# Kernel optimization log

Measured on AMD Instinct MI355X. Metric: run time of the kernel, lower is better.

The kernel has to match this reference:

```python
import jax, jax.numpy as jnp
import numpy as np

N, E, IN, H, OUT = 50000, 1600000, 128, 128, 16


def setup_inputs() -> dict:
    key = jax.random.key(0)
    ks = jax.random.split(key, 8)
    return {
        "x": jax.random.normal(ks[0], (N, IN), dtype=jnp.float32),
        "edge_index": jax.random.randint(ks[1], (2, E), 0, N, dtype=jnp.int64),
        "W1": jax.random.normal(ks[2], (IN, H), dtype=jnp.float32) * 0.05,
        "b1": jax.random.normal(ks[3], (H,), dtype=jnp.float32) * 0.05,
        "W2": jax.random.normal(ks[4], (H, H), dtype=jnp.float32) * 0.05,
        "b2": jax.random.normal(ks[5], (H,), dtype=jnp.float32) * 0.05,
        "Wc": jax.random.normal(ks[6], (H, OUT), dtype=jnp.float32) * 0.05,
        "bc": jax.random.normal(ks[7], (OUT,), dtype=jnp.float32) * 0.05,
    }


def _gcn_conv(x, src, dst, norm, W, b, n):
    # PyG GCNConv: h = x @ W; out[i] = sum_{(j->i)} norm_e * h[j]; out += b
    h = x @ W
    msg = h[src] * norm[:, None]          # [E+N, H] gather + scale
    out = jax.ops.segment_sum(msg, dst, num_segments=n)  # scatter-add
    return out + b


def reference(x, edge_index, W1, b1, W2, b2, Wc, bc):
    n = x.shape[0]
    loop = jnp.arange(n, dtype=edge_index.dtype)
    src = jnp.concatenate([edge_index[0], loop])  # add self-loops
    dst = jnp.concatenate([edge_index[1], loop])
    # symmetric normalization: deg over destinations (incl. self-loops)
    deg = jnp.zeros((n,), dtype=x.dtype).at[dst].add(1.0)
    d_inv_sqrt = jnp.where(deg > 0, jax.lax.rsqrt(deg), 0.0)
    norm = d_inv_sqrt[src] * d_inv_sqrt[dst]
    h = jax.nn.relu(_gcn_conv(x, src, dst, norm, W1, b1, n))
    # dropout p=0.5 is identity in eval mode
    h = jax.nn.relu(_gcn_conv(h, src, dst, norm, W2, b2, n))
    return h @ Wc + bc
```

## Files before the change

### kernel.cpp

```cpp
#include <hip/hip_runtime.h>
#include <hip/hip_bf16.h>


typedef unsigned int uint;
typedef unsigned short ushort;
typedef __attribute__((ext_vector_type(8))) short bf16x8;
typedef __attribute__((ext_vector_type(4))) float f32x4;

#define NPB 256
#define MAXBKT 256
#define CAP 12288

static __device__ __forceinline__ ushort f2bf(float f) {
    unsigned u = __float_as_uint(f);
    u += 0x7fffu + ((u >> 16) & 1u);
    return (ushort)(u >> 16);
}
static __device__ __forceinline__ uint pack2(float a, float b) {
    return (uint)f2bf(a) | ((uint)f2bf(b) << 16);
}
static __device__ __forceinline__ float lo2f(uint u) { return __uint_as_float(u << 16); }
static __device__ __forceinline__ float hi2f(uint u) { return __uint_as_float(u & 0xffff0000u); }

#define UNPACK8(dst, u)                                        \
    dst[0] = lo2f(u.x); dst[1] = hi2f(u.x);                    \
    dst[2] = lo2f(u.y); dst[3] = hi2f(u.y);                    \
    dst[4] = lo2f(u.z); dst[5] = hi2f(u.z);                    \
    dst[6] = lo2f(u.w); dst[7] = hi2f(u.w);


__global__ __launch_bounds__(256) void initcur(int* __restrict__ bcursor, int nbuckets) {
    int t = threadIdx.x;
    if (t < nbuckets) bcursor[t] = t * CAP;
}

__global__ __launch_bounds__(256) void bin_edges(const int* __restrict__ src,
                                                 const int* __restrict__ dst,
                                                 int* __restrict__ bcursor,
                                                 uint* __restrict__ pay,
                                                 int E, int nbuckets) {
    __shared__ int h[MAXBKT];
    __shared__ int base[MAXBKT];
    int tid = threadIdx.x;
    h[tid] = 0;
    __syncthreads();
    int chunk = (E + gridDim.x - 1) / gridDim.x;
    int i0 = blockIdx.x * chunk;
    int i1 = min(E, i0 + chunk);
    for (int i = i0 + tid; i < i1; i += 256) atomicAdd(&h[dst[i] >> 8], 1);
    __syncthreads();
    if (tid < nbuckets) base[tid] = h[tid] ? atomicAdd(&bcursor[tid], h[tid]) : 0;
    __syncthreads();
    h[tid] = 0;
    __syncthreads();
    for (int i = i0 + tid; i < i1; i += 256) {
        int d = dst[i];
        int b = d >> 8;
        int pos = base[b] + atomicAdd(&h[b], 1);
        pay[pos] = (uint)src[i] | ((uint)(d & 255) << 24);
    }
}

__global__ __launch_bounds__(256) void build_rows(const uint* __restrict__ pay,
                                                  const int* __restrict__ bcursor,
                                                  int* __restrict__ rowstart,
                                                  int* __restrict__ rowend,
                                                  float* __restrict__ dinv,
                                                  int* __restrict__ colidx, int n) {
    __shared__ int hist[NPB];
    __shared__ int sc[NPB];
    __shared__ int cur[NPB];
    int tid = threadIdx.x;
    int b = blockIdx.x;
    int node0 = b * NPB;
    int s = b * CAP, e = bcursor[b];

    hist[tid] = 0;
    __syncthreads();
    for (int i = s + tid; i < e; i += 256) atomicAdd(&hist[pay[i] >> 24], 1);
    __syncthreads();

    int v = hist[tid];
    sc[tid] = v;
    __syncthreads();
    for (int d = 1; d < 256; d <<= 1) {
        int x = (tid >= d) ? sc[tid - d] : 0;
        __syncthreads();
        sc[tid] += x;
        __syncthreads();
    }
    int excl = sc[tid] - v;
    cur[tid] = s + excl;
    int node = node0 + tid;
    if (node < n) {
        rowstart[node] = s + excl;
        rowend[node] = s + excl + v;
        dinv[node] = rsqrtf((float)(v + 1));
    }
    __syncthreads();

    for (int i = s + tid; i < e; i += 256) {
        uint p = pay[i];
        int pos = atomicAdd(&cur[p >> 24], 1);
        colidx[pos] = (int)(p & 0xffffffu);
    }
}

__global__ __launch_bounds__(256) void prep_wt(const float* __restrict__ W1,
                                               const float* __restrict__ W2,
                                               ushort* __restrict__ Wt1,
                                               ushort* __restrict__ Wt2) {
    int idx = blockIdx.x * 256 + threadIdx.x;
    int k = idx >> 7, nn = idx & 127;
    Wt1[nn * 128 + k] = f2bf(W1[idx]);
    Wt2[nn * 128 + k] = f2bf(W2[idx]);
}

template <bool A_BF16>
__global__ __launch_bounds__(256) void gemm_mfma(const void* __restrict__ Xv,
                                                 const ushort* __restrict__ Wt,
                                                 const float* __restrict__ dinv,
                                                 uint* __restrict__ Yb, int n) {
    __shared__ __align__(16) ushort sOut[4][16][136];
    const int wave = threadIdx.x >> 6;
    const int lane = threadIdx.x & 63;
    const int quad = lane >> 4, l16 = lane & 15;
    const int m0 = blockIdx.x * 64 + wave * 16;

    f32x4 acc[8];
#pragma unroll
    for (int t = 0; t < 8; ++t) acc[t] = (f32x4){0.f, 0.f, 0.f, 0.f};

    int arow = m0 + l16;
    arow = arow < n ? arow : n - 1;

#pragma unroll
    for (int ks = 0; ks < 4; ++ks) {
        bf16x8 a;
        if (A_BF16) {
            const ushort* X = (const ushort*)Xv;
            a = *(const bf16x8*)&X[(size_t)arow * 128 + ks * 32 + quad * 8];
        } else {
            const float* X = (const float*)Xv;
            const float* px = &X[(size_t)arow * 128 + ks * 32 + quad * 8];
            float4 x0 = *(const float4*)px;
            float4 x1 = *(const float4*)(px + 4);
            ushort av[8] = {f2bf(x0.x), f2bf(x0.y), f2bf(x0.z), f2bf(x0.w),
                            f2bf(x1.x), f2bf(x1.y), f2bf(x1.z), f2bf(x1.w)};
            a = *(const bf16x8*)av;
        }
#pragma unroll
        for (int nt = 0; nt < 8; ++nt) {
            bf16x8 b = *(const bf16x8*)&Wt[(size_t)(nt * 16 + l16) * 128 + ks * 32 + quad * 8];
            acc[nt] = __builtin_amdgcn_mfma_f32_16x16x32_bf16(a, b, acc[nt], 0, 0, 0);
        }
    }

    float dv[4];
#pragma unroll
    for (int r = 0; r < 4; ++r) {
        int rr = m0 + quad * 4 + r;
        dv[r] = dinv[rr < n ? rr : n - 1];
    }
#pragma unroll
    for (int nt = 0; nt < 8; ++nt)
#pragma unroll
        for (int r = 0; r < 4; ++r)
            sOut[wave][quad * 4 + r][nt * 16 + l16] = f2bf(acc[nt][r] * dv[r]);
    __syncthreads();

#pragma unroll
    for (int i = 0; i < 4; ++i) {
        int linear = i * 64 + lane;
        int row = linear >> 4, chunk = linear & 15;
        int rr = m0 + row;
        if (rr < n) {
            uint4 v = *(const uint4*)&sOut[wave][row][chunk * 8];
            *(uint4*)&Yb[(size_t)rr * 64 + chunk * 4] = v;
        }
    }
}

static __device__ __forceinline__ void gather_q(const uint4* __restrict__ H4,
                                                int s, int e, int nn, int sub,
                                                const int* __restrict__ colidx,
                                                float acc[8]) {
    uint4 su = H4[(size_t)nn * 16 + sub];
    float t[8];
    UNPACK8(t, su);
#pragma unroll
    for (int j = 0; j < 8; ++j) acc[j] = t[j];

    int p = s;
    for (; p + 8 <= e; p += 8) {
        int c[8];
#pragma unroll
        for (int i = 0; i < 8; ++i) c[i] = colidx[p + i];
        uint4 u[8];
#pragma unroll
        for (int i = 0; i < 8; ++i) u[i] = H4[(size_t)c[i] * 16 + sub];
#pragma unroll
        for (int i = 0; i < 8; ++i) {
            float a[8];
            UNPACK8(a, u[i]);
#pragma unroll
            for (int j = 0; j < 8; ++j) acc[j] += a[j];
        }
    }
    if (p < e) {
        int c[8];
#pragma unroll
        for (int i = 0; i < 8; ++i) c[i] = (p + i < e) ? colidx[p + i] : nn;
        uint4 u[8];
#pragma unroll
        for (int i = 0; i < 8; ++i) u[i] = H4[(size_t)c[i] * 16 + sub];
#pragma unroll
        for (int i = 0; i < 8; ++i) {
            float a[8];
            UNPACK8(a, u[i]);
#pragma unroll
            for (int j = 0; j < 8; ++j) acc[j] += a[j];
        }
        float pad = (float)(p + 8 - e);
#pragma unroll
        for (int j = 0; j < 8; ++j) acc[j] -= pad * t[j];
    }
}

__global__ __launch_bounds__(256) void agg_mid_q(const uint4* __restrict__ H4,
                                                 const int* __restrict__ rowstart,
                                                 const int* __restrict__ rowend,
                                                 const int* __restrict__ colidx,
                                                 const float* __restrict__ dinv,
                                                 const float* __restrict__ bias,
                                                 uint4* __restrict__ Ob, int n) {
    int tid = threadIdx.x;
    int sub = tid & 15;
    int node = blockIdx.x * 16 + (tid >> 4);
    int nn = node < n ? node : n - 1;
    int s = rowstart[nn], e = rowend[nn];
    float di = dinv[nn];

    float acc[8];
    gather_q(H4, s, e, nn, sub, colidx, acc);

    if (node < n) {
        float4 b0 = ((const float4*)bias)[sub * 2];
        float4 b1 = ((const float4*)bias)[sub * 2 + 1];
        float o0 = fmaxf(fmaf(acc[0], di, b0.x), 0.f);
        float o1 = fmaxf(fmaf(acc[1], di, b0.y), 0.f);
        float o2 = fmaxf(fmaf(acc[2], di, b0.z), 0.f);
        float o3 = fmaxf(fmaf(acc[3], di, b0.w), 0.f);
        float o4 = fmaxf(fmaf(acc[4], di, b1.x), 0.f);
        float o5 = fmaxf(fmaf(acc[5], di, b1.y), 0.f);
        float o6 = fmaxf(fmaf(acc[6], di, b1.z), 0.f);
        float o7 = fmaxf(fmaf(acc[7], di, b1.w), 0.f);
        uint4 ov;
        ov.x = pack2(o0, o1); ov.y = pack2(o2, o3);
        ov.z = pack2(o4, o5); ov.w = pack2(o6, o7);
        Ob[(size_t)node * 16 + sub] = ov;
    }
}

__global__ __launch_bounds__(256) void agg_out_q(const uint4* __restrict__ H4,
                                                 const int* __restrict__ rowstart,
                                                 const int* __restrict__ rowend,
                                                 const int* __restrict__ colidx,
                                                 const float* __restrict__ dinv,
                                                 const float* __restrict__ bias,
                                                 const float* __restrict__ Wc,
                                                 const float* __restrict__ bc,
                                                 float* __restrict__ out, int n) {
    __shared__ float sA[16][129];
    int tid = threadIdx.x;
    int sub = tid & 15;
    int nl = tid >> 4;
    int node = blockIdx.x * 16 + nl;
    int nn = node < n ? node : n - 1;
    int s = rowstart[nn], e = rowend[nn];
    float di = dinv[nn];

    float acc[8];
    gather_q(H4, s, e, nn, sub, colidx, acc);

    {
        float4 b0 = ((const float4*)bias)[sub * 2];
        float4 b1 = ((const float4*)bias)[sub * 2 + 1];
        float f[8];
        f[0] = fmaxf(fmaf(acc[0], di, b0.x), 0.f);
        f[1] = fmaxf(fmaf(acc[1], di, b0.y), 0.f);
        f[2] = fmaxf(fmaf(acc[2], di, b0.z), 0.f);
        f[3] = fmaxf(fmaf(acc[3], di, b0.w), 0.f);
        f[4] = fmaxf(fmaf(acc[4], di, b1.x), 0.f);
        f[5] = fmaxf(fmaf(acc[5], di, b1.y), 0.f);
        f[6] = fmaxf(fmaf(acc[6], di, b1.z), 0.f);
        f[7] = fmaxf(fmaf(acc[7], di, b1.w), 0.f);
#pragma unroll
        for (int j = 0; j < 8; ++j) sA[nl][sub * 8 + j] = f[j];
    }
    __syncthreads();

    int col = tid & 15;
    float p0 = 0.f, p1 = 0.f;
#pragma unroll 4
    for (int k = 0; k < 128; k += 2) {
        p0 = fmaf(sA[nl][k], Wc[k * 16 + col], p0);
        p1 = fmaf(sA[nl][k + 1], Wc[(k + 1) * 16 + col], p1);
    }
    if (node < n) out[(size_t)node * 16 + col] = p0 + p1 + bc[col];
}


extern "C" void kernel_launch(void* const* d_in, const int* in_sizes, int n_in,
                              void* d_out, int out_size, void* d_ws, size_t ws_size,
                              hipStream_t stream) {
    const float* x  = (const float*)d_in[0];
    const int*   ei = (const int*)d_in[1];
    const float* W1 = (const float*)d_in[2];
    const float* b1 = (const float*)d_in[3];
    const float* W2 = (const float*)d_in[4];
    const float* b2 = (const float*)d_in[5];
    const float* Wc = (const float*)d_in[6];
    const float* bc = (const float*)d_in[7];
    float* out = (float*)d_out;

    const int n = in_sizes[0] / 128;
    const int E = in_sizes[1] / 2;
    const int* src = ei;
    const int* dst = ei + E;
    const int nbuckets = (n + NPB - 1) / NPB;

    char* p = (char*)d_ws;
    auto alloc = [&](size_t bytes) {
        char* q = p;
        p += (bytes + 255) & ~(size_t)255;
        return q;
    };
    int*    bcursor  = (int*)alloc(MAXBKT * 4);
    int*    rowstart = (int*)alloc((size_t)n * 4);
    int*    rowend   = (int*)alloc((size_t)n * 4);
    float*  dinv     = (float*)alloc((size_t)n * 4);
    ushort* Wt1      = (ushort*)alloc(128 * 128 * 2);
    ushort* Wt2      = (ushort*)alloc(128 * 128 * 2);
    uint*   pay      = (uint*)alloc((size_t)nbuckets * CAP * 4);
    int*    colidx   = (int*)alloc((size_t)nbuckets * CAP * 4);
    uint*   bufA     = (uint*)alloc((size_t)n * 64 * 4);
    uint*   bufB     = (uint*)alloc((size_t)n * 64 * 4);
    if ((size_t)(p - (char*)d_ws) > ws_size) return;

    initcur<<<1, 256, 0, stream>>>(bcursor, nbuckets);
    bin_edges<<<256, 256, 0, stream>>>(src, dst, bcursor, pay, E, nbuckets);
    build_rows<<<nbuckets, 256, 0, stream>>>(pay, bcursor, rowstart, rowend, dinv, colidx, n);
    prep_wt<<<64, 256, 0, stream>>>(W1, W2, Wt1, Wt2);

    const int gemmb = (n + 63) / 64;
    const int aggb = (n + 15) / 16;
    gemm_mfma<false><<<gemmb, 256, 0, stream>>>(x, Wt1, dinv, bufA, n);
    agg_mid_q<<<aggb, 256, 0, stream>>>((const uint4*)bufA, rowstart, rowend, colidx,
                                        dinv, b1, (uint4*)bufB, n);
    gemm_mfma<true><<<gemmb, 256, 0, stream>>>(bufB, Wt2, dinv, bufA, n);
    agg_out_q<<<aggb, 256, 0, stream>>>((const uint4*)bufA, rowstart, rowend, colidx,
                                        dinv, b2, Wc, bc, out, n);
}
```

Baseline: 284.8 us.

## Fuse all GCN stages into one persistent cooperative kernel with grid syncs

Replaces the eight separate launches (cursor init, binning, row build, weight prep, two GEMMs, two aggregations) with one cooperative kernel of 512 persistent blocks. Stages are separated by grid-wide barriers, and each stage loops over its tiles or buckets in grid-stride fashion. Shared memory is unioned across the phases. This removes launch overhead and inter-kernel gaps, but the binning stage now uses 512 edge chunks instead of 256. It also adds grid-sync costs, fixes the grid size so occupancy may be limited, and makes the aggregation blocks loop with extra block barriers.

Result: slower. 675.6 us (+137.2%).

```diff
diff --git a/kernel.cpp b/kernel.cpp
--- a/kernel.cpp
+++ b/kernel.cpp
@@ -1,6 +1,9 @@
 #include <hip/hip_runtime.h>
 #include <hip/hip_bf16.h>
-
+#include <hip/hip_cooperative_groups.h>
+
+
+namespace cg = cooperative_groups;
 
 typedef unsigned int uint;
 typedef unsigned short ushort;
@@ -8,8 +11,8 @@
 typedef __attribute__((ext_vector_type(4))) float f32x4;
 
 #define NPB 256
-#define MAXBKT 256
 #define CAP 12288
+#define GRID 512
 
 static __device__ __forceinline__ ushort f2bf(float f) {
     unsigned u = __float_as_uint(f);
@@ -28,158 +31,36 @@
     dst[4] = lo2f(u.z); dst[5] = hi2f(u.z);                    \
     dst[6] = lo2f(u.w); dst[7] = hi2f(u.w);
 
-
-__global__ __launch_bounds__(256) void initcur(int* __restrict__ bcursor, int nbuckets) {
-    int t = threadIdx.x;
-    if (t < nbuckets) bcursor[t] = t * CAP;
-}
-
-__global__ __launch_bounds__(256) void bin_edges(const int* __restrict__ src,
-                                                 const int* __restrict__ dst,
-                                                 int* __restrict__ bcursor,
-                                                 uint* __restrict__ pay,
-                                                 int E, int nbuckets) {
-    __shared__ int h[MAXBKT];
-    __shared__ int base[MAXBKT];
-    int tid = threadIdx.x;
-    h[tid] = 0;
-    __syncthreads();
-    int chunk = (E + gridDim.x - 1) / gridDim.x;
-    int i0 = blockIdx.x * chunk;
-    int i1 = min(E, i0 + chunk);
-    for (int i = i0 + tid; i < i1; i += 256) atomicAdd(&h[dst[i] >> 8], 1);
-    __syncthreads();
-    if (tid < nbuckets) base[tid] = h[tid] ? atomicAdd(&bcursor[tid], h[tid]) : 0;
-    __syncthreads();
-    h[tid] = 0;
-    __syncthreads();
-    for (int i = i0 + tid; i < i1; i += 256) {
-        int d = dst[i];
-        int b = d >> 8;
-        int pos = base[b] + atomicAdd(&h[b], 1);
-        pay[pos] = (uint)src[i] | ((uint)(d & 255) << 24);
-    }
-}
-
-__global__ __launch_bounds__(256) void build_rows(const uint* __restrict__ pay,
-                                                  const int* __restrict__ bcursor,
-                                                  int* __restrict__ rowstart,
-                                                  int* __restrict__ rowend,
-                                                  float* __restrict__ dinv,
-                                                  int* __restrict__ colidx, int n) {
-    __shared__ int hist[NPB];
-    __shared__ int sc[NPB];
-    __shared__ int cur[NPB];
-    int tid = threadIdx.x;
-    int b = blockIdx.x;
-    int node0 = b * NPB;
-    int s = b * CAP, e = bcursor[b];
-
-    hist[tid] = 0;
-    __syncthreads();
-    for (int i = s + tid; i < e; i += 256) atomicAdd(&hist[pay[i] >> 24], 1);
-    __syncthreads();
-
-    int v = hist[tid];
-    sc[tid] = v;
-    __syncthreads();
-    for (int d = 1; d < 256; d <<= 1) {
-        int x = (tid >= d) ? sc[tid - d] : 0;
-        __syncthreads();
-        sc[tid] += x;
-        __syncthreads();
-    }
-    int excl = sc[tid] - v;
-    cur[tid] = s + excl;
-    int node = node0 + tid;
-    if (node < n) {
-        rowstart[node] = s + excl;
-        rowend[node] = s + excl + v;
-        dinv[node] = rsqrtf((float)(v + 1));
-    }
-    __syncthreads();
-
-    for (int i = s + tid; i < e; i += 256) {
-        uint p = pay[i];
-        int pos = atomicAdd(&cur[p >> 24], 1);
-        colidx[pos] = (int)(p & 0xffffffu);
-    }
-}
-
-__global__ __launch_bounds__(256) void prep_wt(const float* __restrict__ W1,
-                                               const float* __restrict__ W2,
-                                               ushort* __restrict__ Wt1,
-                                               ushort* __restrict__ Wt2) {
-    int idx = blockIdx.x * 256 + threadIdx.x;
-    int k = idx >> 7, nn = idx & 127;
-    Wt1[nn * 128 + k] = f2bf(W1[idx]);
-    Wt2[nn * 128 + k] = f2bf(W2[idx]);
-}
-
-template <bool A_BF16>
-__global__ __launch_bounds__(256) void gemm_mfma(const void* __restrict__ Xv,
-                                                 const ushort* __restrict__ Wt,
-                                                 const float* __restrict__ dinv,
-                                                 uint* __restrict__ Yb, int n) {
-    __shared__ __align__(16) ushort sOut[4][16][136];
-    const int wave = threadIdx.x >> 6;
-    const int lane = threadIdx.x & 63;
-    const int quad = lane >> 4, l16 = lane & 15;
-    const int m0 = blockIdx.x * 64 + wave * 16;
-
-    f32x4 acc[8];
-#pragma unroll
-    for (int t = 0; t < 8; ++t) acc[t] = (f32x4){0.f, 0.f, 0.f, 0.f};
-
-    int arow = m0 + l16;
-    arow = arow < n ? arow : n - 1;
-
-#pragma unroll
-    for (int ks = 0; ks < 4; ++ks) {
-        bf16x8 a;
-        if (A_BF16) {
-            const ushort* X = (const ushort*)Xv;
-            a = *(const bf16x8*)&X[(size_t)arow * 128 + ks * 32 + quad * 8];
-        } else {
-            const float* X = (const float*)Xv;
-            const float* px = &X[(size_t)arow * 128 + ks * 32 + quad * 8];
-            float4 x0 = *(const float4*)px;
-            float4 x1 = *(const float4*)(px + 4);
-            ushort av[8] = {f2bf(x0.x), f2bf(x0.y), f2bf(x0.z), f2bf(x0.w),
-                            f2bf(x1.x), f2bf(x1.y), f2bf(x1.z), f2bf(x1.w)};
-            a = *(const bf16x8*)av;
-        }
-#pragma unroll
-        for (int nt = 0; nt < 8; ++nt) {
-            bf16x8 b = *(const bf16x8*)&Wt[(size_t)(nt * 16 + l16) * 128 + ks * 32 + quad * 8];
-            acc[nt] = __builtin_amdgcn_mfma_f32_16x16x32_bf16(a, b, acc[nt], 0, 0, 0);
-        }
-    }
-
-    float dv[4];
-#pragma unroll
-    for (int r = 0; r < 4; ++r) {
-        int rr = m0 + quad * 4 + r;
-        dv[r] = dinv[rr < n ? rr : n - 1];
-    }
-#pragma unroll
-    for (int nt = 0; nt < 8; ++nt)
-#pragma unroll
-        for (int r = 0; r < 4; ++r)
-            sOut[wave][quad * 4 + r][nt * 16 + l16] = f2bf(acc[nt][r] * dv[r]);
-    __syncthreads();
-
-#pragma unroll
-    for (int i = 0; i < 4; ++i) {
-        int linear = i * 64 + lane;
-        int row = linear >> 4, chunk = linear & 15;
-        int rr = m0 + row;
-        if (rr < n) {
-            uint4 v = *(const uint4*)&sOut[wave][row][chunk * 8];
-            *(uint4*)&Yb[(size_t)rr * 64 + chunk * 4] = v;
-        }
-    }
-}
+struct Params {
+    const float* x;
+    const int* src;
+    const int* dst;
+    const float* W1;
+    const float* b1;
+    const float* W2;
+    const float* b2;
+    const float* Wc;
+    const float* bc;
+    float* out;
+    int* bcursor;
+    int* rowstart;
+    int* rowend;
+    float* dinv;
+    ushort* Wt1;
+    ushort* Wt2;
+    uint* pay;
+    int* colidx;
+    uint* bufA;
+    uint* bufB;
+    int n, E, nbuckets, ntile64, ntile16;
+};
+
+union __align__(16) SharedU {
+    struct { int h[256]; int base[256]; } bin;
+    struct { int hist[256]; int sc[256]; int cur[256]; } br;
+    ushort sOut[4][16][136];
+    float sA[16][129];
+};
 
 static __device__ __forceinline__ void gather_q(const uint4* __restrict__ H4,
                                                 int s, int e, int nn, int sub,
@@ -227,107 +108,225 @@
     }
 }
 
-__global__ __launch_bounds__(256) void agg_mid_q(const uint4* __restrict__ H4,
-                                                 const int* __restrict__ rowstart,
-                                                 const int* __restrict__ rowend,
-                                                 const int* __restrict__ colidx,
-                                                 const float* __restrict__ dinv,
-                                                 const float* __restrict__ bias,
-                                                 uint4* __restrict__ Ob, int n) {
-    int tid = threadIdx.x;
-    int sub = tid & 15;
-    int node = blockIdx.x * 16 + (tid >> 4);
-    int nn = node < n ? node : n - 1;
-    int s = rowstart[nn], e = rowend[nn];
-    float di = dinv[nn];
-
-    float acc[8];
-    gather_q(H4, s, e, nn, sub, colidx, acc);
-
-    if (node < n) {
-        float4 b0 = ((const float4*)bias)[sub * 2];
-        float4 b1 = ((const float4*)bias)[sub * 2 + 1];
-        float o0 = fmaxf(fmaf(acc[0], di, b0.x), 0.f);
-        float o1 = fmaxf(fmaf(acc[1], di, b0.y), 0.f);
-        float o2 = fmaxf(fmaf(acc[2], di, b0.z), 0.f);
-        float o3 = fmaxf(fmaf(acc[3], di, b0.w), 0.f);
-        float o4 = fmaxf(fmaf(acc[4], di, b1.x), 0.f);
-        float o5 = fmaxf(fmaf(acc[5], di, b1.y), 0.f);
-        float o6 = fmaxf(fmaf(acc[6], di, b1.z), 0.f);
-        float o7 = fmaxf(fmaf(acc[7], di, b1.w), 0.f);
-        uint4 ov;
-        ov.x = pack2(o0, o1); ov.y = pack2(o2, o3);
-        ov.z = pack2(o4, o5); ov.w = pack2(o6, o7);
-        Ob[(size_t)node * 16 + sub] = ov;
-    }
-}
-
-__global__ __launch_bounds__(256) void agg_out_q(const uint4* __restrict__ H4,
-                                                 const int* __restrict__ rowstart,
-                                                 const int* __restrict__ rowend,
-                                                 const int* __restrict__ colidx,
-                                                 const float* __restrict__ dinv,
-                                                 const float* __restrict__ bias,
-                                                 const float* __restrict__ Wc,
-                                                 const float* __restrict__ bc,
-                                                 float* __restrict__ out, int n) {
-    __shared__ float sA[16][129];
-    int tid = threadIdx.x;
-    int sub = tid & 15;
-    int nl = tid >> 4;
-    int node = blockIdx.x * 16 + nl;
-    int nn = node < n ? node : n - 1;
-    int s = rowstart[nn], e = rowend[nn];
-    float di = dinv[nn];
-
-    float acc[8];
-    gather_q(H4, s, e, nn, sub, colidx, acc);
+template <bool A_BF16>
+static __device__ __forceinline__ void gemm_phase(const Params& P, SharedU& sm,
+                                                  const void* Xv,
+                                                  const ushort* Wt, uint* Yb) {
+    const int wave = threadIdx.x >> 6;
+    const int lane = threadIdx.x & 63;
+    const int quad = lane >> 4, l16 = lane & 15;
+
+    for (int t = blockIdx.x; t < P.ntile64; t += GRID) {
+        const int m0 = t * 64 + wave * 16;
+        f32x4 acc[8];
+#pragma unroll
+        for (int i = 0; i < 8; ++i) acc[i] = (f32x4){0.f, 0.f, 0.f, 0.f};
+
+        int arow = m0 + l16;
+        arow = arow < P.n ? arow : P.n - 1;
+
+#pragma unroll
+        for (int ks = 0; ks < 4; ++ks) {
+            bf16x8 a;
+            if (A_BF16) {
+                const ushort* X = (const ushort*)Xv;
+                a = *(const bf16x8*)&X[(size_t)arow * 128 + ks * 32 + quad * 8];
+            } else {
+                const float* X = (const float*)Xv;
+                const float* px = &X[(size_t)arow * 128 + ks * 32 + quad * 8];
+                float4 x0 = *(const float4*)px;
+                float4 x1 = *(const float4*)(px + 4);
+                ushort av[8] = {f2bf(x0.x), f2bf(x0.y), f2bf(x0.z), f2bf(x0.w),
+                                f2bf(x1.x), f2bf(x1.y), f2bf(x1.z), f2bf(x1.w)};
+                a = *(const bf16x8*)av;
+            }
+#pragma unroll
+            for (int nt = 0; nt < 8; ++nt) {
+                bf16x8 b = *(const bf16x8*)&Wt[(size_t)(nt * 16 + l16) * 128 + ks * 32 + quad * 8];
+                acc[nt] = __builtin_amdgcn_mfma_f32_16x16x32_bf16(a, b, acc[nt], 0, 0, 0);
+            }
+        }
+
+        float dv[4];
+#pragma unroll
+        for (int r = 0; r < 4; ++r) {
+            int rr = m0 + quad * 4 + r;
+            dv[r] = P.dinv[rr < P.n ? rr : P.n - 1];
+        }
+        __syncthreads();
+#pragma unroll
+        for (int nt = 0; nt < 8; ++nt)
+#pragma unroll
+            for (int r = 0; r < 4; ++r)
+                sm.sOut[wave][quad * 4 + r][nt * 16 + l16] = f2bf(acc[nt][r] * dv[r]);
+        __syncthreads();
+
+#pragma unroll
+        for (int i = 0; i < 4; ++i) {
+            int linear = i * 64 + lane;
+            int row = linear >> 4, chunk = linear & 15;
+            int rr = m0 + row;
+            if (rr < P.n) {
+                uint4 v = *(const uint4*)&sm.sOut[wave][row][chunk * 8];
+                *(uint4*)&Yb[(size_t)rr * 64 + chunk * 4] = v;
+            }
+        }
+    }
+}
+
+__global__ __launch_bounds__(256, 2) void gcn_all(Params P) {
+    cg::grid_group gridg = cg::this_grid();
+    __shared__ SharedU sm;
+    const int tid = threadIdx.x;
+    const int bid = blockIdx.x;
+    const int gid = bid * 256 + tid;
+
+    if (gid < P.nbuckets) P.bcursor[gid] = gid * CAP;
+    for (int idx = gid; idx < 128 * 128; idx += GRID * 256) {
+        int k = idx >> 7, nn = idx & 127;
+        P.Wt1[nn * 128 + k] = f2bf(P.W1[idx]);
+        P.Wt2[nn * 128 + k] = f2bf(P.W2[idx]);
+    }
+    gridg.sync();
 
     {
-        float4 b0 = ((const float4*)bias)[sub * 2];
-        float4 b1 = ((const float4*)bias)[sub * 2 + 1];
-        float f[8];
-        f[0] = fmaxf(fmaf(acc[0], di, b0.x), 0.f);
-        f[1] = fmaxf(fmaf(acc[1], di, b0.y), 0.f);
-        f[2] = fmaxf(fmaf(acc[2], di, b0.z), 0.f);
-        f[3] = fmaxf(fmaf(acc[3], di, b0.w), 0.f);
-        f[4] = fmaxf(fmaf(acc[4], di, b1.x), 0.f);
-        f[5] = fmaxf(fmaf(acc[5], di, b1.y), 0.f);
-        f[6] = fmaxf(fmaf(acc[6], di, b1.z), 0.f);
-        f[7] = fmaxf(fmaf(acc[7], di, b1.w), 0.f);
-#pragma unroll
-        for (int j = 0; j < 8; ++j) sA[nl][sub * 8 + j] = f[j];
-    }
-    __syncthreads();
-
-    int col = tid & 15;
-    float p0 = 0.f, p1 = 0.f;
+        sm.bin.h[tid] = 0;
+        __syncthreads();
+        int chunk = (P.E + GRID - 1) / GRID;
+        int i0 = bid * chunk;
+        int i1 = min(P.E, i0 + chunk);
+        for (int i = i0 + tid; i < i1; i += 256) atomicAdd(&sm.bin.h[P.dst[i] >> 8], 1);
+        __syncthreads();
+        if (tid < P.nbuckets)
+            sm.bin.base[tid] = sm.bin.h[tid] ? atomicAdd(&P.bcursor[tid], sm.bin.h[tid]) : 0;
+        __syncthreads();
+        sm.bin.h[tid] = 0;
+        __syncthreads();
+        for (int i = i0 + tid; i < i1; i += 256) {
+            int d = P.dst[i];
+            int b = d >> 8;
+            int pos = sm.bin.base[b] + atomicAdd(&sm.bin.h[b], 1);
+            P.pay[pos] = (uint)P.src[i] | ((uint)(d & 255) << 24);
+        }
+    }
+    gridg.sync();
+
+    for (int b = bid; b < P.nbuckets; b += GRID) {
+        int node0 = b * NPB;
+        int s = b * CAP, e = P.bcursor[b];
+        sm.br.hist[tid] = 0;
+        __syncthreads();
+        for (int i = s + tid; i < e; i += 256) atomicAdd(&sm.br.hist[P.pay[i] >> 24], 1);
+        __syncthreads();
+        int v = sm.br.hist[tid];
+        sm.br.sc[tid] = v;
+        __syncthreads();
+        for (int d = 1; d < 256; d <<= 1) {
+            int xx = (tid >= d) ? sm.br.sc[tid - d] : 0;
+            __syncthreads();
+            sm.br.sc[tid] += xx;
+            __syncthreads();
+        }
+        int excl = sm.br.sc[tid] - v;
+        sm.br.cur[tid] = s + excl;
+        int node = node0 + tid;
+        if (node < P.n) {
+            P.rowstart[node] = s + excl;
+            P.rowend[node] = s + excl + v;
+            P.dinv[node] = rsqrtf((float)(v + 1));
+        }
+        __syncthreads();
+        for (int i = s + tid; i < e; i += 256) {
+            uint pp = P.pay[i];
+            int pos = atomicAdd(&sm.br.cur[pp >> 24], 1);
+            P.colidx[pos] = (int)(pp & 0xffffffu);
+        }
+        __syncthreads();
+    }
+    gridg.sync();
+
+    gemm_phase<false>(P, sm, P.x, P.Wt1, P.bufA);
+    gridg.sync();
+
+    {
+        const uint4* H4 = (const uint4*)P.bufA;
+        uint4* Ob = (uint4*)P.bufB;
+        int sub = tid & 15;
+        int nl = tid >> 4;
+        for (int blk = bid; blk < P.ntile16; blk += GRID) {
+            int node = blk * 16 + nl;
+            int nn = node < P.n ? node : P.n - 1;
+            int s = P.rowstart[nn], e = P.rowend[nn];
+            float di = P.dinv[nn];
+            float acc[8];
+            gather_q(H4, s, e, nn, sub, P.colidx, acc);
+            if (node < P.n) {
+                float4 b0 = ((const float4*)P.b1)[sub * 2];
+                float4 b1v = ((const float4*)P.b1)[sub * 2 + 1];
+                uint4 ov;
+                ov.x = pack2(fmaxf(fmaf(acc[0], di, b0.x), 0.f),
+                             fmaxf(fmaf(acc[1], di, b0.y), 0.f));
+                ov.y = pack2(fmaxf(fmaf(acc[2], di, b0.z), 0.f),
+                             fmaxf(fmaf(acc[3], di, b0.w), 0.f));
+                ov.z = pack2(fmaxf(fmaf(acc[4], di, b1v.x), 0.f),
+                             fmaxf(fmaf(acc[5], di, b1v.y), 0.f));
+                ov.w = pack2(fmaxf(fmaf(acc[6], di, b1v.z), 0.f),
+                             fmaxf(fmaf(acc[7], di, b1v.w), 0.f));
+                Ob[(size_t)node * 16 + sub] = ov;
+            }
+        }
+    }
+    gridg.sync();
+
+    gemm_phase<true>(P, sm, P.bufB, P.Wt2, P.bufA);
+    gridg.sync();
+
+    {
+        const uint4* H4 = (const uint4*)P.bufA;
+        int sub = tid & 15;
+        int nl = tid >> 4;
+        for (int blk = bid; blk < P.ntile16; blk += GRID) {
+            int node = blk * 16 + nl;
+            int nn = node < P.n ? node : P.n - 1;
+            int s = P.rowstart[nn], e = P.rowend[nn];
+            float di = P.dinv[nn];
+            float acc[8];
+            gather_q(H4, s, e, nn, sub, P.colidx, acc);
+
+            float4 b0 = ((const float4*)P.b2)[sub * 2];
+            float4 b1v = ((const float4*)P.b2)[sub * 2 + 1];
+            float f[8];
+            f[0] = fmaxf(fmaf(acc[0], di, b0.x), 0.f);
+            f[1] = fmaxf(fmaf(acc[1], di, b0.y), 0.f);
+            f[2] = fmaxf(fmaf(acc[2], di, b0.z), 0.f);
+            f[3] = fmaxf(fmaf(acc[3], di, b0.w), 0.f);
+            f[4] = fmaxf(fmaf(acc[4], di, b1v.x), 0.f);
+            f[5] = fmaxf(fmaf(acc[5], di, b1v.y), 0.f);
+            f[6] = fmaxf(fmaf(acc[6], di, b1v.z), 0.f);
+            f[7] = fmaxf(fmaf(acc[7], di, b1v.w), 0.f);
+            __syncthreads();
+#pragma unroll
+            for (int j = 0; j < 8; ++j) sm.sA[nl][sub * 8 + j] = f[j];
+            __syncthreads();
+
+            int col = tid & 15;
+            float p0 = 0.f, p1 = 0.f;
 #pragma unroll 4
-    for (int k = 0; k < 128; k += 2) {
-        p0 = fmaf(sA[nl][k], Wc[k * 16 + col], p0);
-        p1 = fmaf(sA[nl][k + 1], Wc[(k + 1) * 16 + col], p1);
-    }
-    if (node < n) out[(size_t)node * 16 + col] = p0 + p1 + bc[col];
+            for (int k = 0; k < 128; k += 2) {
+                p0 = fmaf(sm.sA[nl][k], P.Wc[k * 16 + col], p0);
+                p1 = fmaf(sm.sA[nl][k + 1], P.Wc[(k + 1) * 16 + col], p1);
+            }
+            if (node < P.n) P.out[(size_t)node * 16 + col] = p0 + p1 + P.bc[col];
+        }
+    }
 }
 
 
 extern "C" void kernel_launch(void* const* d_in, const int* in_sizes, int n_in,
                               void* d_out, int out_size, void* d_ws, size_t ws_size,
                               hipStream_t stream) {
-    const float* x  = (const float*)d_in[0];
-    const int*   ei = (const int*)d_in[1];
-    const float* W1 = (const float*)d_in[2];
-    const float* b1 = (const float*)d_in[3];
-    const float* W2 = (const float*)d_in[4];
-    const float* b2 = (const float*)d_in[5];
-    const float* Wc = (const float*)d_in[6];
-    const float* bc = (const float*)d_in[7];
-    float* out = (float*)d_out;
-
     const int n = in_sizes[0] / 128;
     const int E = in_sizes[1] / 2;
-    const int* src = ei;
-    const int* dst = ei + E;
     const int nbuckets = (n + NPB - 1) / NPB;
 
     char* p = (char*)d_ws;
@@ -336,7 +335,7 @@
         p += (bytes + 255) & ~(size_t)255;
         return q;
     };
-    int*    bcursor  = (int*)alloc(MAXBKT * 4);
+    int*    bcursor  = (int*)alloc(256 * 4);
     int*    rowstart = (int*)alloc((size_t)n * 4);
     int*    rowend   = (int*)alloc((size_t)n * 4);
     float*  dinv     = (float*)alloc((size_t)n * 4);
@@ -348,17 +347,33 @@
     uint*   bufB     = (uint*)alloc((size_t)n * 64 * 4);
     if ((size_t)(p - (char*)d_ws) > ws_size) return;
 
-    initcur<<<1, 256, 0, stream>>>(bcursor, nbuckets);
-    bin_edges<<<256, 256, 0, stream>>>(src, dst, bcursor, pay, E, nbuckets);
-    build_rows<<<nbuckets, 256, 0, stream>>>(pay, bcursor, rowstart, rowend, dinv, colidx, n);
-    prep_wt<<<64, 256, 0, stream>>>(W1, W2, Wt1, Wt2);
-
-    const int gemmb = (n + 63) / 64;
-    const int aggb = (n + 15) / 16;
-    gemm_mfma<false><<<gemmb, 256, 0, stream>>>(x, Wt1, dinv, bufA, n);
-    agg_mid_q<<<aggb, 256, 0, stream>>>((const uint4*)bufA, rowstart, rowend, colidx,
-                                        dinv, b1, (uint4*)bufB, n);
-    gemm_mfma<true><<<gemmb, 256, 0, stream>>>(bufB, Wt2, dinv, bufA, n);
-    agg_out_q<<<aggb, 256, 0, stream>>>((const uint4*)bufA, rowstart, rowend, colidx,
-                                        dinv, b2, Wc, bc, out, n);
-}
+    Params prm;
+    prm.x  = (const float*)d_in[0];
+    prm.src = (const int*)d_in[1];
+    prm.dst = (const int*)d_in[1] + E;
+    prm.W1 = (const float*)d_in[2];
+    prm.b1 = (const float*)d_in[3];
+    prm.W2 = (const float*)d_in[4];
+    prm.b2 = (const float*)d_in[5];
+    prm.Wc = (const float*)d_in[6];
+    prm.bc = (const float*)d_in[7];
+    prm.out = (float*)d_out;
+    prm.bcursor = bcursor;
+    prm.rowstart = rowstart;
+    prm.rowend = rowend;
+    prm.dinv = dinv;
+    prm.Wt1 = Wt1;
+    prm.Wt2 = Wt2;
+    prm.pay = pay;
+    prm.colidx = colidx;
+    prm.bufA = bufA;
+    prm.bufB = bufB;
+    prm.n = n;
+    prm.E = E;
+    prm.nbuckets = nbuckets;
+    prm.ntile64 = (n + 63) / 64;
+    prm.ntile16 = (n + 15) / 16;
+
+    void* kargs[] = { &prm };
+    hipLaunchCooperativeKernel((void*)gcn_all, dim3(GRID), dim3(256), kargs, 0, stream);
+}
```

## Fuse setup kernels, overlap CSR build with GEMM1, fuse GEMM2 into aggregation

Applied to the files above, without the earlier changes.

Merges the cursor init and weight transpose into one setup kernel that also zeroes a new global degree array. bin_edges now counts degrees with global atomics, so GEMM1 can run in the same grid as the CSR row build: one set of blocks builds the CSR while the others do the GEMM with dinv computed from deg. The second GEMM is fused into the first aggregation kernel using a per-block 16-row MFMA tile, so the intermediate layer-1 activation no longer goes through global memory. This cuts launches and one full activation round trip, at the cost of 1.6M global atomics on deg and a small, lower-occupancy MFMA tile inside the aggregation.

Result: slower. 315.6 us (+10.8%).

```diff
diff --git a/kernel.cpp b/kernel.cpp
--- a/kernel.cpp
+++ b/kernel.cpp
@@ -8,7 +8,6 @@
 typedef __attribute__((ext_vector_type(4))) float f32x4;
 
 #define NPB 256
-#define MAXBKT 256
 #define CAP 12288
 
 static __device__ __forceinline__ ushort f2bf(float f) {
@@ -28,26 +27,42 @@
     dst[4] = lo2f(u.z); dst[5] = hi2f(u.z);                    \
     dst[6] = lo2f(u.w); dst[7] = hi2f(u.w);
 
-
-__global__ __launch_bounds__(256) void initcur(int* __restrict__ bcursor, int nbuckets) {
-    int t = threadIdx.x;
-    if (t < nbuckets) bcursor[t] = t * CAP;
+__global__ __launch_bounds__(256) void setup(int* __restrict__ bcursor,
+                                             int* __restrict__ deg,
+                                             const float* __restrict__ W1,
+                                             const float* __restrict__ W2,
+                                             ushort* __restrict__ Wt1,
+                                             ushort* __restrict__ Wt2,
+                                             int n, int nbuckets) {
+    int gid = blockIdx.x * 256 + threadIdx.x;
+    if (gid < nbuckets) bcursor[gid] = gid * CAP;
+    for (int i = gid; i < n; i += 64 * 256) deg[i] = 0;
+    {
+        int k = gid >> 7, nn = gid & 127;
+        Wt1[nn * 128 + k] = f2bf(W1[gid]);
+        Wt2[nn * 128 + k] = f2bf(W2[gid]);
+    }
 }
 
 __global__ __launch_bounds__(256) void bin_edges(const int* __restrict__ src,
                                                  const int* __restrict__ dst,
                                                  int* __restrict__ bcursor,
+                                                 int* __restrict__ deg,
                                                  uint* __restrict__ pay,
                                                  int E, int nbuckets) {
-    __shared__ int h[MAXBKT];
-    __shared__ int base[MAXBKT];
+    __shared__ int h[256];
+    __shared__ int base[256];
     int tid = threadIdx.x;
     h[tid] = 0;
     __syncthreads();
     int chunk = (E + gridDim.x - 1) / gridDim.x;
     int i0 = blockIdx.x * chunk;
     int i1 = min(E, i0 + chunk);
-    for (int i = i0 + tid; i < i1; i += 256) atomicAdd(&h[dst[i] >> 8], 1);
+    for (int i = i0 + tid; i < i1; i += 256) {
+        int d = dst[i];
+        atomicAdd(&h[d >> 8], 1);
+        atomicAdd(&deg[d], 1);
+    }
     __syncthreads();
     if (tid < nbuckets) base[tid] = h[tid] ? atomicAdd(&bcursor[tid], h[tid]) : 0;
     __syncthreads();
@@ -61,122 +76,105 @@
     }
 }
 
-__global__ __launch_bounds__(256) void build_rows(const uint* __restrict__ pay,
-                                                  const int* __restrict__ bcursor,
-                                                  int* __restrict__ rowstart,
-                                                  int* __restrict__ rowend,
-                                                  float* __restrict__ dinv,
-                                                  int* __restrict__ colidx, int n) {
-    __shared__ int hist[NPB];
-    __shared__ int sc[NPB];
-    __shared__ int cur[NPB];
+__global__ __launch_bounds__(256) void build_gemm1(const uint* __restrict__ pay,
+                                                   const int* __restrict__ bcursor,
+                                                   int* __restrict__ rowstart,
+                                                   int* __restrict__ rowend,
+                                                   float* __restrict__ dinv,
+                                                   int* __restrict__ colidx,
+                                                   const float* __restrict__ x,
+                                                   const ushort* __restrict__ Wt1,
+                                                   const int* __restrict__ deg,
+                                                   uint* __restrict__ bufA,
+                                                   int n, int nbuckets) {
+    __shared__ int s_hist[256];
+    __shared__ int s_sc[256];
+    __shared__ int s_cur[256];
+    __shared__ __align__(16) ushort sOut[4][16][136];
     int tid = threadIdx.x;
-    int b = blockIdx.x;
-    int node0 = b * NPB;
-    int s = b * CAP, e = bcursor[b];
-
-    hist[tid] = 0;
-    __syncthreads();
-    for (int i = s + tid; i < e; i += 256) atomicAdd(&hist[pay[i] >> 24], 1);
-    __syncthreads();
-
-    int v = hist[tid];
-    sc[tid] = v;
-    __syncthreads();
-    for (int d = 1; d < 256; d <<= 1) {
-        int x = (tid >= d) ? sc[tid - d] : 0;
+
+    if ((int)blockIdx.x < nbuckets) {
+        int b = blockIdx.x;
+        int node0 = b * NPB;
+        int s = b * CAP, e = bcursor[b];
+        s_hist[tid] = 0;
         __syncthreads();
-        sc[tid] += x;
+        for (int i = s + tid; i < e; i += 256) atomicAdd(&s_hist[pay[i] >> 24], 1);
         __syncthreads();
-    }
-    int excl = sc[tid] - v;
-    cur[tid] = s + excl;
-    int node = node0 + tid;
-    if (node < n) {
-        rowstart[node] = s + excl;
-        rowend[node] = s + excl + v;
-        dinv[node] = rsqrtf((float)(v + 1));
-    }
-    __syncthreads();
-
-    for (int i = s + tid; i < e; i += 256) {
-        uint p = pay[i];
-        int pos = atomicAdd(&cur[p >> 24], 1);
-        colidx[pos] = (int)(p & 0xffffffu);
-    }
-}
-
-__global__ __launch_bounds__(256) void prep_wt(const float* __restrict__ W1,
-                                               const float* __restrict__ W2,
-                                               ushort* __restrict__ Wt1,
-                                               ushort* __restrict__ Wt2) {
-    int idx = blockIdx.x * 256 + threadIdx.x;
-    int k = idx >> 7, nn = idx & 127;
-    Wt1[nn * 128 + k] = f2bf(W1[idx]);
-    Wt2[nn * 128 + k] = f2bf(W2[idx]);
-}
-
-template <bool A_BF16>
-__global__ __launch_bounds__(256) void gemm_mfma(const void* __restrict__ Xv,
-                                                 const ushort* __restrict__ Wt,
-                                                 const float* __restrict__ dinv,
-                                                 uint* __restrict__ Yb, int n) {
-    __shared__ __align__(16) ushort sOut[4][16][136];
-    const int wave = threadIdx.x >> 6;
-    const int lane = threadIdx.x & 63;
-    const int quad = lane >> 4, l16 = lane & 15;
-    const int m0 = blockIdx.x * 64 + wave * 16;
-
-    f32x4 acc[8];
-#pragma unroll
-    for (int t = 0; t < 8; ++t) acc[t] = (f32x4){0.f, 0.f, 0.f, 0.f};
-
-    int arow = m0 + l16;
-    arow = arow < n ? arow : n - 1;
-
-#pragma unroll
-    for (int ks = 0; ks < 4; ++ks) {
-        bf16x8 a;
-        if (A_BF16) {
-            const ushort* X = (const ushort*)Xv;
-            a = *(const bf16x8*)&X[(size_t)arow * 128 + ks * 32 + quad * 8];
-        } else {
-            const float* X = (const float*)Xv;
-            const float* px = &X[(size_t)arow * 128 + ks * 32 + quad * 8];
+        int v = s_hist[tid];
+        s_sc[tid] = v;
+        __syncthreads();
+        for (int d = 1; d < 256; d <<= 1) {
+            int xx = (tid >= d) ? s_sc[tid - d] : 0;
+            __syncthreads();
+            s_sc[tid] += xx;
+            __syncthreads();
+        }
+        int excl = s_sc[tid] - v;
+        s_cur[tid] = s + excl;
+        int node = node0 + tid;
+        if (node < n) {
+            rowstart[node] = s + excl;
+            rowend[node] = s + excl + v;
+            dinv[node] = rsqrtf((float)(v + 1));
+        }
+        __syncthreads();
+        for (int i = s + tid; i < e; i += 256) {
+            uint pp = pay[i];
+            int pos = atomicAdd(&s_cur[pp >> 24], 1);
+            colidx[pos] = (int)(pp & 0xffffffu);
+        }
+    } else {
+        const int t = blockIdx.x - nbuckets;
+        const int wave = tid >> 6;
+        const int lane = tid & 63;
+        const int quad = lane >> 4, l16 = lane & 15;
+        const int m0 = t * 64 + wave * 16;
+
+        f32x4 acc[8];
+#pragma unroll
+        for (int i = 0; i < 8; ++i) acc[i] = (f32x4){0.f, 0.f, 0.f, 0.f};
+
+        int arow = m0 + l16;
+        arow = arow < n ? arow : n - 1;
+
+#pragma unroll
+        for (int ks = 0; ks < 4; ++ks) {
+            const float* px = &x[(size_t)arow * 128 + ks * 32 + quad * 8];
             float4 x0 = *(const float4*)px;
             float4 x1 = *(const float4*)(px + 4);
             ushort av[8] = {f2bf(x0.x), f2bf(x0.y), f2bf(x0.z), f2bf(x0.w),
                             f2bf(x1.x), f2bf(x1.y), f2bf(x1.z), f2bf(x1.w)};
-            a = *(const bf16x8*)av;
-        }
-#pragma unroll
-        for (int nt = 0; nt < 8; ++nt) {
-            bf16x8 b = *(const bf16x8*)&Wt[(size_t)(nt * 16 + l16) * 128 + ks * 32 + quad * 8];
-            acc[nt] = __builtin_amdgcn_mfma_f32_16x16x32_bf16(a, b, acc[nt], 0, 0, 0);
-        }
-    }
-
-    float dv[4];
-#pragma unroll
-    for (int r = 0; r < 4; ++r) {
-        int rr = m0 + quad * 4 + r;
-        dv[r] = dinv[rr < n ? rr : n - 1];
-    }
-#pragma unroll
-    for (int nt = 0; nt < 8; ++nt)
-#pragma unroll
-        for (int r = 0; r < 4; ++r)
-            sOut[wave][quad * 4 + r][nt * 16 + l16] = f2bf(acc[nt][r] * dv[r]);
-    __syncthreads();
-
-#pragma unroll
-    for (int i = 0; i < 4; ++i) {
-        int linear = i * 64 + lane;
-        int row = linear >> 4, chunk = linear & 15;
-        int rr = m0 + row;
-        if (rr < n) {
-            uint4 v = *(const uint4*)&sOut[wave][row][chunk * 8];
-            *(uint4*)&Yb[(size_t)rr * 64 + chunk * 4] = v;
+            bf16x8 a = *(const bf16x8*)av;
+#pragma unroll
+            for (int nt = 0; nt < 8; ++nt) {
+                bf16x8 b = *(const bf16x8*)&Wt1[(size_t)(nt * 16 + l16) * 128 + ks * 32 + quad * 8];
+                acc[nt] = __builtin_amdgcn_mfma_f32_16x16x32_bf16(a, b, acc[nt], 0, 0, 0);
+            }
+        }
+
+        float dv[4];
+#pragma unroll
+        for (int r = 0; r < 4; ++r) {
+            int rr = m0 + quad * 4 + r;
+            dv[r] = rsqrtf((float)(deg[rr < n ? rr : n - 1] + 1));
+        }
+#pragma unroll
+        for (int nt = 0; nt < 8; ++nt)
+#pragma unroll
+            for (int r = 0; r < 4; ++r)
+                sOut[wave][quad * 4 + r][nt * 16 + l16] = f2bf(acc[nt][r] * dv[r]);
+        __syncthreads();
+
+#pragma unroll
+        for (int i = 0; i < 4; ++i) {
+            int linear = i * 64 + lane;
+            int row = linear >> 4, chunk = linear & 15;
+            int rr = m0 + row;
+            if (rr < n) {
+                uint4 v = *(const uint4*)&sOut[wave][row][chunk * 8];
+                *(uint4*)&bufA[(size_t)rr * 64 + chunk * 4] = v;
+            }
         }
     }
 }
@@ -227,38 +225,78 @@
     }
 }
 
-__global__ __launch_bounds__(256) void agg_mid_q(const uint4* __restrict__ H4,
+__global__ __launch_bounds__(256) void agg_gemm2(const uint4* __restrict__ H4,
                                                  const int* __restrict__ rowstart,
                                                  const int* __restrict__ rowend,
                                                  const int* __restrict__ colidx,
                                                  const float* __restrict__ dinv,
-                                                 const float* __restrict__ bias,
-                                                 uint4* __restrict__ Ob, int n) {
+                                                 const float* __restrict__ b1,
+                                                 const ushort* __restrict__ Wt2,
+                                                 uint* __restrict__ Yb, int n) {
+    __shared__ __align__(16) ushort sA[16][136];
+    __shared__ __align__(16) ushort sO[16][136];
     int tid = threadIdx.x;
     int sub = tid & 15;
-    int node = blockIdx.x * 16 + (tid >> 4);
+    int nl = tid >> 4;
+    int node0 = blockIdx.x * 16;
+    int node = node0 + nl;
     int nn = node < n ? node : n - 1;
     int s = rowstart[nn], e = rowend[nn];
     float di = dinv[nn];
 
     float acc[8];
     gather_q(H4, s, e, nn, sub, colidx, acc);
-
-    if (node < n) {
-        float4 b0 = ((const float4*)bias)[sub * 2];
-        float4 b1 = ((const float4*)bias)[sub * 2 + 1];
-        float o0 = fmaxf(fmaf(acc[0], di, b0.x), 0.f);
-        float o1 = fmaxf(fmaf(acc[1], di, b0.y), 0.f);
-        float o2 = fmaxf(fmaf(acc[2], di, b0.z), 0.f);
-        float o3 = fmaxf(fmaf(acc[3], di, b0.w), 0.f);
-        float o4 = fmaxf(fmaf(acc[4], di, b1.x), 0.f);
-        float o5 = fmaxf(fmaf(acc[5], di, b1.y), 0.f);
-        float o6 = fmaxf(fmaf(acc[6], di, b1.z), 0.f);
-        float o7 = fmaxf(fmaf(acc[7], di, b1.w), 0.f);
-        uint4 ov;
-        ov.x = pack2(o0, o1); ov.y = pack2(o2, o3);
-        ov.z = pack2(o4, o5); ov.w = pack2(o6, o7);
-        Ob[(size_t)node * 16 + sub] = ov;
+    {
+        float4 c0 = ((const float4*)b1)[sub * 2];
+        float4 c1 = ((const float4*)b1)[sub * 2 + 1];
+        float f0 = fmaxf(fmaf(acc[0], di, c0.x), 0.f);
+        float f1 = fmaxf(fmaf(acc[1], di, c0.y), 0.f);
+        float f2 = fmaxf(fmaf(acc[2], di, c0.z), 0.f);
+        float f3 = fmaxf(fmaf(acc[3], di, c0.w), 0.f);
+        float f4 = fmaxf(fmaf(acc[4], di, c1.x), 0.f);
+        float f5 = fmaxf(fmaf(acc[5], di, c1.y), 0.f);
+        float f6 = fmaxf(fmaf(acc[6], di, c1.z), 0.f);
+        float f7 = fmaxf(fmaf(acc[7], di, c1.w), 0.f);
+        uint4 v;
+        v.x = pack2(f0, f1); v.y = pack2(f2, f3);
+        v.z = pack2(f4, f5); v.w = pack2(f6, f7);
+        *(uint4*)&sA[nl][sub * 8] = v;
+    }
+    __syncthreads();
+
+    const int wave = tid >> 6;
+    const int lane = tid & 63;
+    const int quad = lane >> 4, l16 = lane & 15;
+    f32x4 acc2[2];
+    acc2[0] = (f32x4){0.f, 0.f, 0.f, 0.f};
+    acc2[1] = (f32x4){0.f, 0.f, 0.f, 0.f};
+#pragma unroll
+    for (int ks = 0; ks < 4; ++ks) {
+        bf16x8 a = *(const bf16x8*)&sA[l16][ks * 32 + quad * 8];
+#pragma unroll
+        for (int t = 0; t < 2; ++t) {
+            int nt = wave * 2 + t;
+            bf16x8 b = *(const bf16x8*)&Wt2[(size_t)(nt * 16 + l16) * 128 + ks * 32 + quad * 8];
+            acc2[t] = __builtin_amdgcn_mfma_f32_16x16x32_bf16(a, b, acc2[t], 0, 0, 0);
+        }
+    }
+#pragma unroll
+    for (int r = 0; r < 4; ++r) {
+        int rr = node0 + quad * 4 + r;
+        float dv = dinv[rr < n ? rr : n - 1];
+#pragma unroll
+        for (int t = 0; t < 2; ++t)
+            sO[quad * 4 + r][(wave * 2 + t) * 16 + l16] = f2bf(acc2[t][r] * dv);
+    }
+    __syncthreads();
+
+    {
+        int row = tid >> 4, chunk = tid & 15;
+        int rr = node0 + row;
+        if (rr < n) {
+            uint4 v = *(const uint4*)&sO[row][chunk * 8];
+            *(uint4*)&Yb[(size_t)rr * 64 + chunk * 4] = v;
+        }
     }
 }
 
@@ -285,16 +323,16 @@
 
     {
         float4 b0 = ((const float4*)bias)[sub * 2];
-        float4 b1 = ((const float4*)bias)[sub * 2 + 1];
+        float4 b1v = ((const float4*)bias)[sub * 2 + 1];
         float f[8];
         f[0] = fmaxf(fmaf(acc[0], di, b0.x), 0.f);
         f[1] = fmaxf(fmaf(acc[1], di, b0.y), 0.f);
         f[2] = fmaxf(fmaf(acc[2], di, b0.z), 0.f);
         f[3] = fmaxf(fmaf(acc[3], di, b0.w), 0.f);
-        f[4] = fmaxf(fmaf(acc[4], di, b1.x), 0.f);
-        f[5] = fmaxf(fmaf(acc[5], di, b1.y), 0.f);
-        f[6] = fmaxf(fmaf(acc[6], di, b1.z), 0.f);
-        f[7] = fmaxf(fmaf(acc[7], di, b1.w), 0.f);
+        f[4] = fmaxf(fmaf(acc[4], di, b1v.x), 0.f);
+        f[5] = fmaxf(fmaf(acc[5], di, b1v.y), 0.f);
+        f[6] = fmaxf(fmaf(acc[6], di, b1v.z), 0.f);
+        f[7] = fmaxf(fmaf(acc[7], di, b1v.w), 0.f);
 #pragma unroll
         for (int j = 0; j < 8; ++j) sA[nl][sub * 8 + j] = f[j];
     }
@@ -336,7 +374,8 @@
         p += (bytes + 255) & ~(size_t)255;
         return q;
     };
-    int*    bcursor  = (int*)alloc(MAXBKT * 4);
+    int*    bcursor  = (int*)alloc(256 * 4);
+    int*    deg      = (int*)alloc((size_t)n * 4);
     int*    rowstart = (int*)alloc((size_t)n * 4);
     int*    rowend   = (int*)alloc((size_t)n * 4);
     float*  dinv     = (float*)alloc((size_t)n * 4);
@@ -348,17 +387,16 @@
     uint*   bufB     = (uint*)alloc((size_t)n * 64 * 4);
     if ((size_t)(p - (char*)d_ws) > ws_size) return;
 
-    initcur<<<1, 256, 0, stream>>>(bcursor, nbuckets);
-    bin_edges<<<256, 256, 0, stream>>>(src, dst, bcursor, pay, E, nbuckets);
-    build_rows<<<nbuckets, 256, 0, stream>>>(pay, bcursor, rowstart, rowend, dinv, colidx, n);
-    prep_wt<<<64, 256, 0, stream>>>(W1, W2, Wt1, Wt2);
-
-    const int gemmb = (n + 63) / 64;
+    const int ntile64 = (n + 63) / 64;
     const int aggb = (n + 15) / 16;
-    gemm_mfma<false><<<gemmb, 256, 0, stream>>>(x, Wt1, dinv, bufA, n);
-    agg_mid_q<<<aggb, 256, 0, stream>>>((const uint4*)bufA, rowstart, rowend, colidx,
-                                        dinv, b1, (uint4*)bufB, n);
-    gemm_mfma<true><<<gemmb, 256, 0, stream>>>(bufB, Wt2, dinv, bufA, n);
-    agg_out_q<<<aggb, 256, 0, stream>>>((const uint4*)bufA, rowstart, rowend, colidx,
+
+    setup<<<64, 256, 0, stream>>>(bcursor, deg, W1, W2, Wt1, Wt2, n, nbuckets);
+    bin_edges<<<256, 256, 0, stream>>>(src, dst, bcursor, deg, pay, E, nbuckets);
+    build_gemm1<<<nbuckets + ntile64, 256, 0, stream>>>(pay, bcursor, rowstart, rowend,
+                                                        dinv, colidx, x, Wt1, deg, bufA,
+                                                        n, nbuckets);
+    agg_gemm2<<<aggb, 256, 0, stream>>>((const uint4*)bufA, rowstart, rowend, colidx,
+                                        dinv, b1, Wt2, bufB, n);
+    agg_out_q<<<aggb, 256, 0, stream>>>((const uint4*)bufB, rowstart, rowend, colidx,
                                         dinv, b2, Wc, bc, out, n);
 }
```
